# Optimization experiments

Measured on AMD Instinct MI355X. Metric: run time of the kernel, lower is better.

The kernel has to match this reference:

```python
import jax, jax.numpy as jnp
import numpy as np

N, F = 4096, 256
EPS = 1e-12

def _prep_P(P):
    # replicate __init__ preprocessing: symmetrize, normalize, *4, clamp, /4
    P = P + P.T
    P = P / np.sum(P)
    P = P * 4
    P = np.maximum(P, 1e-12)
    P = P / 4
    return P


def setup_inputs() -> dict:
    key = jax.random.key(0)
    k1, k2, k3, k4, k5 = jax.random.split(key, 5)
    rng = np.random.default_rng(0)
    P1 = jnp.asarray(_prep_P(rng.uniform(size=(N, N)).astype(np.float32)))
    P2 = jnp.asarray(_prep_P(rng.uniform(size=(N, N)).astype(np.float32)))
    X1 = jax.random.normal(k1, (N, F), dtype=jnp.float32)
    X2 = jax.random.normal(k2, (N, F), dtype=jnp.float32)
    W = jax.random.uniform(k3, (1, F), dtype=jnp.float32)
    return {"P1": P1, "P2": P2, "X1": X1, "X2": X2, "W": W}


def _batch_loss(P, X, W):
    Y = X * W                                  # [N, F]
    sq = jnp.sum(Y * Y, axis=1)                # [N]
    # squared euclidean distance via mm (matches cdist use_mm_for_euclid_dist, then squared)
    d2 = jnp.maximum(sq[:, None] + sq[None, :] - 2.0 * (Y @ Y.T), 0.0)  # [N, N]
    temp = 1.0 / (1.0 + d2)                    # t-distribution kernel
    n = temp.shape[0]
    diag = jnp.eye(n, dtype=bool)
    temp = jnp.where(diag, 0.0, temp)
    Q = jnp.maximum(temp / jnp.sum(temp), EPS)
    kl = jnp.where(diag, 0.0, P * jnp.log(P / Q))
    return jnp.sum(kl)


def reference(P1, P2, X1, X2, W):
    loss = _batch_loss(P1, X1, W) + _batch_loss(P2, X2, W)
    return loss / 2.0
```

## Files before the change

### kernel.cpp

```cpp
#include <hip/hip_runtime.h>
#include <math.h>

#define N 4096
#define F 256
#define NT 32
#define BM 128

typedef short short8 __attribute__((ext_vector_type(8)));
typedef float f32x4  __attribute__((ext_vector_type(4)));

typedef const __attribute__((address_space(1))) unsigned int guint_t;
typedef __attribute__((address_space(3))) unsigned int luint_t;

__device__ __forceinline__ void gload_lds16(const void* g, void* l) {
    __builtin_amdgcn_global_load_lds((guint_t*)g, (luint_t*)l, 16, 0, 0);
}

__device__ __forceinline__ unsigned short f2bf(float x) {
    unsigned u = __float_as_uint(x);
    unsigned r = (u + 0x7fff + ((u >> 16) & 1)) >> 16;
    return (unsigned short)r;
}
__device__ __forceinline__ float bf2f(unsigned short x) {
    return __uint_as_float(((unsigned)x) << 16);
}

__global__ __launch_bounds__(256)
void prep_kernel(const float* __restrict__ X1, const float* __restrict__ X2,
                 const float* __restrict__ W,
                 unsigned short* __restrict__ Yhi, unsigned short* __restrict__ Ylo,
                 float* __restrict__ sqg)
{
    int row = blockIdx.x & (N - 1);
    int b   = blockIdx.x >> 12;
    const float* X = b ? X2 : X1;
    size_t off = (size_t)b * N * F + (size_t)row * F;
    int t = threadIdx.x;
    float w = W[t];
    float y = X[(size_t)row * F + t] * w;
    unsigned short h = f2bf(y);
    float lf = y - bf2f(h);
    Yhi[off + t] = h;
    Ylo[off + t] = f2bf(lf);
    float s = y * y;
    #pragma unroll
    for (int o = 32; o > 0; o >>= 1) s += __shfl_down(s, o);
    __shared__ float red[4];
    int lane = t & 63, wv = t >> 6;
    if (lane == 0) red[wv] = s;
    __syncthreads();
    if (t == 0) sqg[b * N + row] = red[0] + red[1] + red[2] + red[3];
}

__global__ __launch_bounds__(256)
void tsne_tile_kernel(const unsigned short* __restrict__ Yhi,
                      const unsigned short* __restrict__ Ylo,
                      const float* __restrict__ sqg,
                      const float* __restrict__ P1, const float* __restrict__ P2,
                      double* __restrict__ pS, double* __restrict__ pA,
                      double* __restrict__ pB)
{
    int bx = blockIdx.x, by = blockIdx.y, bz = blockIdx.z;
    int pidx = bz * (NT * NT) + by * NT + bx;
    if (bx < by) {
        if (threadIdx.x == 0) { pS[pidx] = 0.0; pA[pidx] = 0.0; pB[pidx] = 0.0; }
        return;
    }
    const float* P  = bz ? P2 : P1;
    const unsigned short* Ah = Yhi + (size_t)bz * N * F;
    const unsigned short* Al = Ylo + (size_t)bz * N * F;
    const float* sq = sqg + bz * N;
    const float wgt = (bx == by) ? 1.0f : 2.0f;

    __shared__ unsigned short sAh[BM * 32], sAl[BM * 32];
    __shared__ unsigned short sBh[BM * 32], sBl[BM * 32];

    const int t = threadIdx.x;
    const int lane = t & 63, w = t >> 6;
    const int wx = w & 1, wy = w >> 1;

    f32x4 acc[4][4];
    #pragma unroll
    for (int fm = 0; fm < 4; ++fm)
        #pragma unroll
        for (int fn = 0; fn < 4; ++fn) acc[fm][fn] = (f32x4){0.f, 0.f, 0.f, 0.f};

    const int arow = by * BM, brow = bx * BM;
    const int c = lane >> 4, mr = lane & 15;

    for (int k0 = 0; k0 < F; k0 += 32) {
        #pragma unroll
        for (int it = 0; it < 2; ++it) {
            int cid = it * 256 + w * 64 + lane;
            int row = cid >> 2;
            int kl  = cid & 3;
            int kg  = kl ^ (row & 3);
            int ldsoff = (it * 256 + w * 64) * 8;
            size_t ga = (size_t)(arow + row) * F + k0 + kg * 8;
            size_t gb = (size_t)(brow + row) * F + k0 + kg * 8;
            gload_lds16(Ah + ga, &sAh[ldsoff]);
            gload_lds16(Al + ga, &sAl[ldsoff]);
            gload_lds16(Ah + gb, &sBh[ldsoff]);
            gload_lds16(Al + gb, &sBl[ldsoff]);
        }
        __syncthreads();

        short8 ah[4], al[4], bh[4], bl[4];
        #pragma unroll
        for (int fm = 0; fm < 4; ++fm) {
            int row = wy * 64 + fm * 16 + mr;
            int ad = row * 32 + ((c ^ (row & 3)) * 8);
            ah[fm] = *(const short8*)&sAh[ad];
            al[fm] = *(const short8*)&sAl[ad];
        }
        #pragma unroll
        for (int fn = 0; fn < 4; ++fn) {
            int row = wx * 64 + fn * 16 + mr;
            int ad = row * 32 + ((c ^ (row & 3)) * 8);
            bh[fn] = *(const short8*)&sBh[ad];
            bl[fn] = *(const short8*)&sBl[ad];
        }
        #pragma unroll
        for (int fm = 0; fm < 4; ++fm)
            #pragma unroll
            for (int fn = 0; fn < 4; ++fn) {
                acc[fm][fn] = __builtin_amdgcn_mfma_f32_16x16x32_bf16(ah[fm], bh[fn], acc[fm][fn], 0, 0, 0);
                acc[fm][fn] = __builtin_amdgcn_mfma_f32_16x16x32_bf16(ah[fm], bl[fn], acc[fm][fn], 0, 0, 0);
                acc[fm][fn] = __builtin_amdgcn_mfma_f32_16x16x32_bf16(al[fm], bh[fn], acc[fm][fn], 0, 0, 0);
            }
        __syncthreads();
    }

    const int q = lane >> 4, nn = lane & 15;
    const int gi0 = arow + wy * 64, gj0 = brow + wx * 64;
    float sp = 0.f, ap = 0.f, bp = 0.f;
    #pragma unroll
    for (int fm = 0; fm < 4; ++fm) {
        float sqi[4];
        #pragma unroll
        for (int r = 0; r < 4; ++r) sqi[r] = sq[gi0 + fm * 16 + q * 4 + r];
        #pragma unroll
        for (int fn = 0; fn < 4; ++fn) {
            int j = gj0 + fn * 16 + nn;
            float sqj = sq[j];
            #pragma unroll
            for (int r = 0; r < 4; ++r) {
                int i = gi0 + fm * 16 + q * 4 + r;
                float one_d2 = 1.0f + fmaxf(sqi[r] + sqj - 2.0f * acc[fm][fn][r], 0.0f);
                if (i != j) {
                    float p = P[(size_t)i * N + j];
                    sp += __builtin_amdgcn_rcpf(one_d2);
                    ap += p * logf(p * one_d2);
                    bp += p;
                }
            }
        }
    }
    sp *= wgt; ap *= wgt; bp *= wgt;

    #pragma unroll
    for (int o = 32; o > 0; o >>= 1) {
        sp += __shfl_down(sp, o);
        ap += __shfl_down(ap, o);
        bp += __shfl_down(bp, o);
    }
    __shared__ float rS[4], rA[4], rB[4];
    if (lane == 0) { rS[w] = sp; rA[w] = ap; rB[w] = bp; }
    __syncthreads();
    if (t == 0) {
        pS[pidx] = (double)(rS[0] + rS[1] + rS[2] + rS[3]);
        pA[pidx] = (double)(rA[0] + rA[1] + rA[2] + rA[3]);
        pB[pidx] = (double)(rB[0] + rB[1] + rB[2] + rB[3]);
    }
}

__global__ __launch_bounds__(256)
void finish_kernel(const double* __restrict__ pS, const double* __restrict__ pA,
                   const double* __restrict__ pB, float* __restrict__ out)
{
    int t = threadIdx.x;
    double s0 = 0, a0 = 0, b0 = 0, s1 = 0, a1 = 0, b1 = 0;
    for (int i = t; i < NT * NT; i += 256) {
        s0 += pS[i];           a0 += pA[i];           b0 += pB[i];
        s1 += pS[i + NT * NT]; a1 += pA[i + NT * NT]; b1 += pB[i + NT * NT];
    }
    __shared__ double red[6][256];
    red[0][t] = s0; red[1][t] = a0; red[2][t] = b0;
    red[3][t] = s1; red[4][t] = a1; red[5][t] = b1;
    __syncthreads();
    for (int o = 128; o > 0; o >>= 1) {
        if (t < o) {
            #pragma unroll
            for (int qd = 0; qd < 6; ++qd) red[qd][t] += red[qd][t + o];
        }
        __syncthreads();
    }
    if (t == 0) {
        double kl1 = red[1][0] + red[2][0] * log(red[0][0]);
        double kl2 = red[4][0] + red[5][0] * log(red[3][0]);
        out[0] = (float)((kl1 + kl2) * 0.5);
    }
}

extern "C" void kernel_launch(void* const* d_in, const int* in_sizes, int n_in,
                              void* d_out, int out_size, void* d_ws, size_t ws_size,
                              hipStream_t stream)
{
    const float* P1 = (const float*)d_in[0];
    const float* P2 = (const float*)d_in[1];
    const float* X1 = (const float*)d_in[2];
    const float* X2 = (const float*)d_in[3];
    const float* W  = (const float*)d_in[4];
    float* out = (float*)d_out;

    unsigned short* Yhi = (unsigned short*)d_ws;
    unsigned short* Ylo = Yhi + (size_t)2 * N * F;
    float* sq = (float*)(Ylo + (size_t)2 * N * F);
    double* pS = (double*)(sq + 2 * N);
    double* pA = pS + 2 * NT * NT;
    double* pB = pA + 2 * NT * NT;

    prep_kernel<<<2 * N, 256, 0, stream>>>(X1, X2, W, Yhi, Ylo, sq);
    tsne_tile_kernel<<<dim3(NT, NT, 2), 256, 0, stream>>>(Yhi, Ylo, sq,
                                                          P1, P2, pS, pA, pB);
    finish_kernel<<<1, 256, 0, stream>>>(pS, pA, pB, out);
}
```

Before: 231.3 us.

## Double-buffer LDS tiles, change swizzle, fast log, batch rows in prep kernel

The tile kernel now double-buffers the bf16 hi/lo LDS tiles so the next K-slice's global-to-LDS loads are issued before the current slice's MFMAs run, and it changes the XOR swizzle to use (row>>1)&3. The epilogue uses __logf instead of logf and reuses the tile buffer for the final reduction. The prep kernel processes 8 rows per block, launching fewer blocks. Together these aim to hide load latency and cut launch and transcendental overhead, at the cost of doubled LDS use (64KB), which may reduce occupancy, and slightly lower log accuracy.

```diff
diff --git a/kernel.cpp b/kernel.cpp
--- a/kernel.cpp
+++ b/kernel.cpp
@@ -5,6 +5,7 @@
 #define F 256
 #define NT 32
 #define BM 128
+#define BK 32
 
 typedef short short8 __attribute__((ext_vector_type(8)));
 typedef float f32x4  __attribute__((ext_vector_type(4)));
@@ -31,25 +32,31 @@
                  unsigned short* __restrict__ Yhi, unsigned short* __restrict__ Ylo,
                  float* __restrict__ sqg)
 {
-    int row = blockIdx.x & (N - 1);
-    int b   = blockIdx.x >> 12;
-    const float* X = b ? X2 : X1;
-    size_t off = (size_t)b * N * F + (size_t)row * F;
-    int t = threadIdx.x;
-    float w = W[t];
-    float y = X[(size_t)row * F + t] * w;
-    unsigned short h = f2bf(y);
-    float lf = y - bf2f(h);
-    Yhi[off + t] = h;
-    Ylo[off + t] = f2bf(lf);
-    float s = y * y;
-    #pragma unroll
-    for (int o = 32; o > 0; o >>= 1) s += __shfl_down(s, o);
-    __shared__ float red[4];
-    int lane = t & 63, wv = t >> 6;
-    if (lane == 0) red[wv] = s;
-    __syncthreads();
-    if (t == 0) sqg[b * N + row] = red[0] + red[1] + red[2] + red[3];
+    const int t = threadIdx.x;
+    const int rid0 = blockIdx.x * 8;
+    const float w = W[t];
+    __shared__ float red[8][4];
+    const int lane = t & 63, wv = t >> 6;
+    #pragma unroll
+    for (int r = 0; r < 8; ++r) {
+        int rid = rid0 + r;
+        int b = rid >> 12, row = rid & (N - 1);
+        const float* X = b ? X2 : X1;
+        float y = X[(size_t)row * F + t] * w;
+        unsigned short h = f2bf(y);
+        float lf = y - bf2f(h);
+        size_t off = (size_t)rid * F + t;
+        Yhi[off] = h;
+        Ylo[off] = f2bf(lf);
+        float s = y * y;
+        #pragma unroll
+        for (int o = 32; o > 0; o >>= 1) s += __shfl_down(s, o);
+        if (lane == 0) red[r][wv] = s;
+    }
+    __syncthreads();
+    if (t < 8) {
+        sqg[rid0 + t] = red[t][0] + red[t][1] + red[t][2] + red[t][3];
+    }
 }
 
 __global__ __launch_bounds__(256)
@@ -72,8 +79,7 @@
     const float* sq = sqg + bz * N;
     const float wgt = (bx == by) ? 1.0f : 2.0f;
 
-    __shared__ unsigned short sAh[BM * 32], sAl[BM * 32];
-    __shared__ unsigned short sBh[BM * 32], sBl[BM * 32];
+    __shared__ unsigned short sbuf[2][4][BM * BK];
 
     const int t = threadIdx.x;
     const int lane = t & 63, w = t >> 6;
@@ -88,37 +94,45 @@
     const int arow = by * BM, brow = bx * BM;
     const int c = lane >> 4, mr = lane & 15;
 
-    for (int k0 = 0; k0 < F; k0 += 32) {
-        #pragma unroll
-        for (int it = 0; it < 2; ++it) {
-            int cid = it * 256 + w * 64 + lane;
-            int row = cid >> 2;
-            int kl  = cid & 3;
-            int kg  = kl ^ (row & 3);
-            int ldsoff = (it * 256 + w * 64) * 8;
-            size_t ga = (size_t)(arow + row) * F + k0 + kg * 8;
-            size_t gb = (size_t)(brow + row) * F + k0 + kg * 8;
-            gload_lds16(Ah + ga, &sAh[ldsoff]);
-            gload_lds16(Al + ga, &sAl[ldsoff]);
-            gload_lds16(Ah + gb, &sBh[ldsoff]);
-            gload_lds16(Al + gb, &sBl[ldsoff]);
-        }
-        __syncthreads();
+#define STAGE(db, k0)                                                      \
+    {                                                                      \
+        _Pragma("unroll")                                                  \
+        for (int it = 0; it < 2; ++it) {                                   \
+            int cid = it * 256 + w * 64 + lane;                            \
+            int row = cid >> 2;                                            \
+            int kl  = cid & 3;                                             \
+            int kg  = kl ^ ((row >> 1) & 3);                               \
+            int ldsoff = (it * 256 + w * 64) * 8;                          \
+            size_t ga = (size_t)(arow + row) * F + (k0) + kg * 8;          \
+            size_t gb = (size_t)(brow + row) * F + (k0) + kg * 8;          \
+            gload_lds16(Ah + ga, &sbuf[db][0][ldsoff]);                    \
+            gload_lds16(Al + ga, &sbuf[db][1][ldsoff]);                    \
+            gload_lds16(Ah + gb, &sbuf[db][2][ldsoff]);                    \
+            gload_lds16(Al + gb, &sbuf[db][3][ldsoff]);                    \
+        }                                                                  \
+    }
+
+    STAGE(0, 0);
+    __syncthreads();
+
+    for (int ks = 0; ks < F / BK; ++ks) {
+        const int db = ks & 1;
+        if (ks < F / BK - 1) STAGE(db ^ 1, (ks + 1) * BK);
 
         short8 ah[4], al[4], bh[4], bl[4];
         #pragma unroll
         for (int fm = 0; fm < 4; ++fm) {
             int row = wy * 64 + fm * 16 + mr;
-            int ad = row * 32 + ((c ^ (row & 3)) * 8);
-            ah[fm] = *(const short8*)&sAh[ad];
-            al[fm] = *(const short8*)&sAl[ad];
+            int ad = row * BK + ((c ^ ((row >> 1) & 3)) * 8);
+            ah[fm] = *(const short8*)&sbuf[db][0][ad];
+            al[fm] = *(const short8*)&sbuf[db][1][ad];
         }
         #pragma unroll
         for (int fn = 0; fn < 4; ++fn) {
             int row = wx * 64 + fn * 16 + mr;
-            int ad = row * 32 + ((c ^ (row & 3)) * 8);
-            bh[fn] = *(const short8*)&sBh[ad];
-            bl[fn] = *(const short8*)&sBl[ad];
+            int ad = row * BK + ((c ^ ((row >> 1) & 3)) * 8);
+            bh[fn] = *(const short8*)&sbuf[db][2][ad];
+            bl[fn] = *(const short8*)&sbuf[db][3][ad];
         }
         #pragma unroll
         for (int fm = 0; fm < 4; ++fm)
@@ -130,6 +144,7 @@
             }
         __syncthreads();
     }
+#undef STAGE
 
     const int q = lane >> 4, nn = lane & 15;
     const int gi0 = arow + wy * 64, gj0 = brow + wx * 64;
@@ -150,7 +165,7 @@
                 if (i != j) {
                     float p = P[(size_t)i * N + j];
                     sp += __builtin_amdgcn_rcpf(one_d2);
-                    ap += p * logf(p * one_d2);
+                    ap += p * __logf(p * one_d2);
                     bp += p;
                 }
             }
@@ -164,13 +179,13 @@
         ap += __shfl_down(ap, o);
         bp += __shfl_down(bp, o);
     }
-    __shared__ float rS[4], rA[4], rB[4];
-    if (lane == 0) { rS[w] = sp; rA[w] = ap; rB[w] = bp; }
+    float* red = (float*)&sbuf[0][0][0];
+    if (lane == 0) { red[w] = sp; red[4 + w] = ap; red[8 + w] = bp; }
     __syncthreads();
     if (t == 0) {
-        pS[pidx] = (double)(rS[0] + rS[1] + rS[2] + rS[3]);
-        pA[pidx] = (double)(rA[0] + rA[1] + rA[2] + rA[3]);
-        pB[pidx] = (double)(rB[0] + rB[1] + rB[2] + rB[3]);
+        pS[pidx] = (double)(red[0] + red[1] + red[2] + red[3]);
+        pA[pidx] = (double)(red[4] + red[5] + red[6] + red[7]);
+        pB[pidx] = (double)(red[8] + red[9] + red[10] + red[11]);
     }
 }
 
@@ -220,7 +235,7 @@
     double* pA = pS + 2 * NT * NT;
     double* pB = pA + 2 * NT * NT;
 
-    prep_kernel<<<2 * N, 256, 0, stream>>>(X1, X2, W, Yhi, Ylo, sq);
+    prep_kernel<<<(2 * N) / 8, 256, 0, stream>>>(X1, X2, W, Yhi, Ylo, sq);
     tsne_tile_kernel<<<dim3(NT, NT, 2), 256, 0, stream>>>(Yhi, Ylo, sq,
                                                           P1, P2, pS, pA, pB);
     finish_kernel<<<1, 256, 0, stream>>>(pS, pA, pB, out);
```

Result: faster. 221.9 us (-4.1%).
